# Kernel optimization log

Measured on AMD Instinct MI355X. Metric: run time of the kernel, lower is better.

## Reference

```python
import jax, jax.numpy as jnp
import numpy as np
import itertools

N, F, R, O, OUT = 131072, 32, 256, 5, 100
K = 9  # 2*exp_param + 1 with exp_param=4


def setup_inputs() -> dict:
    key = jax.random.key(0)
    k1, k2, k3 = jax.random.split(key, 3)
    # binary features -> get_route(x)==1 -> categorical rule path
    x = jax.random.randint(k1, (N, F), 0, 2).astype(jnp.float32)
    # first R combinations of O feature indices out of F (itertools order, as in __init__)
    combs = np.array(list(itertools.islice(itertools.combinations(range(F), O), R)), dtype=np.int32)
    comb_space = jax.random.normal(k2, (O, R), dtype=jnp.float32)
    w_out = jax.random.normal(k3, (OUT, R), dtype=jnp.float32) * 0.05
    b_out = jnp.zeros((OUT,), jnp.float32)
    return {"x": x, "comb_space": comb_space, "w_out": w_out, "b_out": b_out,
            "comb_idx": jnp.asarray(combs)}


def reference(x, comb_space, w_out, b_out, comb_idx):
    # Fused version of the per-rule Python loop:
    # gather all rule feature subsets at once: [N, R, O]
    gathered = x[:, comb_idx]
    # per-rule dot product with its parameter vector comb_space[:, r]
    scores = jnp.einsum('nro,or->nr', gathered, comb_space)  # [N, R]
    # polyClip activation: clamp(s^k, -1, 1)
    comb_pred = jnp.clip(scores ** K, -1.0, 1.0)
    # dropout p=0.1 is identity in eval mode
    attn = jax.nn.softmax(comb_pred, axis=1)                 # [N, R]
    out = attn @ w_out.T + b_out                             # [N, OUT]
    return jax.nn.log_softmax(out, axis=1)
```

## Files before the change

kernel.cpp:

```cpp
#include <hip/hip_runtime.h>

typedef unsigned short u16;
typedef _Float16 f16;
typedef __attribute__((ext_vector_type(8))) _Float16 f16x8;
typedef __attribute__((ext_vector_type(4))) _Float16 f16x4;
typedef __attribute__((ext_vector_type(4))) float f32x4;

#define N_ROWS 131072
#define FDIM 32
#define RDIM 256
#define ODIM 5
#define NOUT 100
#define JT 7
#define WAVES 8
#define ROWS_PER_BLOCK (WAVES * 2 * 16)
#define NBLOCKS (N_ROWS / ROWS_PER_BLOCK)

__device__ __forceinline__ u16 f2h_bits(float f) {
    f16 h = (f16)f;
    union { f16 h; u16 u; } v; v.h = h;
    return v.u;
}

__global__ void build_mfrag(const float* __restrict__ cs, const int* __restrict__ ci,
                            u16* __restrict__ mf) {
    int t = blockIdx.x * blockDim.x + threadIdx.x;
    if (t >= 16 * 64) return;
    int lane = t & 63;
    int rt = t >> 6;
    int r = rt * 16 + (lane & 15);
    int kbase = (lane >> 4) * 8;
#pragma unroll
    for (int e = 0; e < 8; ++e) {
        int k = kbase + e;
        float v = 0.f;
#pragma unroll
        for (int o = 0; o < ODIM; ++o)
            if (ci[r * ODIM + o] == k) v = cs[o * RDIM + r];
        mf[t * 8 + e] = f2h_bits(v);
    }
}

__global__ void build_wfrag(const float* __restrict__ w, u16* __restrict__ wf) {
    int t = blockIdx.x * blockDim.x + threadIdx.x;
    if (t >= JT * 8 * 64) return;
    int lane = t & 63;
    int ft = t >> 6;
    int jt = ft >> 3, rtp = ft & 7;
    int j = jt * 16 + (lane & 15);
#pragma unroll
    for (int half = 0; half < 2; ++half) {
#pragma unroll
        for (int e = 0; e < 4; ++e) {
            int r = rtp * 32 + half * 16 + (lane >> 4) * 4 + e;
            float v = (j < NOUT) ? w[j * RDIM + r] : ((j == NOUT) ? 1.0f : 0.0f);
            wf[(ft * 64 + lane) * 8 + half * 4 + e] = f2h_bits(v);
        }
    }
}

__device__ __forceinline__ f16x4 elemop(f32x4 cc) {
    f16x4 r;
#pragma unroll
    for (int i = 0; i < 4; ++i) {
        float s = cc[i];
        float s2 = s * s, s4 = s2 * s2, s8 = s4 * s4;
        float p = fminf(fmaxf(s8 * s, -1.f), 1.f);
        r[i] = (f16)__expf(p);
    }
    return r;
}

__device__ __forceinline__ void epilogue(const f32x4* acc, const float* bv,
                                         int rowbase, int c15, int g,
                                         float* __restrict__ out) {
    float rin[4];
#pragma unroll
    for (int i = 0; i < 4; ++i) rin[i] = 1.f / __shfl(acc[6][i], g * 16 + 4, 64);
#pragma unroll
    for (int i = 0; i < 4; ++i) {
        float lg[JT];
        float mx = -3.0e38f;
#pragma unroll
        for (int jt = 0; jt < JT; ++jt) {
            bool valid = (jt < 6) || (c15 < 4);
            lg[jt] = valid ? (acc[jt][i] * rin[i] + bv[jt]) : -3.0e38f;
            mx = fmaxf(mx, lg[jt]);
        }
#pragma unroll
        for (int m = 1; m <= 8; m <<= 1) mx = fmaxf(mx, __shfl_xor(mx, m, 64));
        float se = 0.f;
#pragma unroll
        for (int jt = 0; jt < JT; ++jt) {
            bool valid = (jt < 6) || (c15 < 4);
            if (valid) se += __expf(lg[jt] - mx);
        }
#pragma unroll
        for (int m = 1; m <= 8; m <<= 1) se += __shfl_xor(se, m, 64);
        float lse = __logf(se);
        int row = rowbase + g * 4 + i;
        float* op = out + (size_t)row * NOUT;
#pragma unroll
        for (int jt = 0; jt < JT; ++jt) {
            bool valid = (jt < 6) || (c15 < 4);
            if (valid) op[jt * 16 + c15] = lg[jt] - mx - lse;
        }
    }
}

__global__ __launch_bounds__(WAVES * 64, 2) void hornet_main(
    const float* __restrict__ x, const u16* __restrict__ mfg,
    const u16* __restrict__ wfg, const float* __restrict__ b_out,
    float* __restrict__ out)
{
    __shared__ __align__(16) u16 wf[JT * 8 * 64 * 8];

    const int tid = threadIdx.x;
    const int lane = tid & 63;
    const int wid = tid >> 6;
    const int c15 = lane & 15, g = lane >> 4;

    const int rowb0 = blockIdx.x * ROWS_PER_BLOCK + wid * 32;
    const float* xp0 = x + (size_t)(rowb0 + c15) * FDIM + g * 8;
    float4 x0a = ((const float4*)xp0)[0];
    float4 x0b = ((const float4*)xp0)[1];
    float4 x1a = ((const float4*)(xp0 + 16 * FDIM))[0];
    float4 x1b = ((const float4*)(xp0 + 16 * FDIM))[1];

    {
        const uint4* wsrc = (const uint4*)wfg;
        uint4* wd = (uint4*)wf;
#pragma unroll
        for (int i = 0; i < 7; ++i) wd[tid + i * 512] = wsrc[tid + i * 512];
    }

    f16x8 a1_0, a1_1;
    a1_0[0] = (f16)x0a.x; a1_0[1] = (f16)x0a.y; a1_0[2] = (f16)x0a.z; a1_0[3] = (f16)x0a.w;
    a1_0[4] = (f16)x0b.x; a1_0[5] = (f16)x0b.y; a1_0[6] = (f16)x0b.z; a1_0[7] = (f16)x0b.w;
    a1_1[0] = (f16)x1a.x; a1_1[1] = (f16)x1a.y; a1_1[2] = (f16)x1a.z; a1_1[3] = (f16)x1a.w;
    a1_1[4] = (f16)x1b.x; a1_1[5] = (f16)x1b.y; a1_1[6] = (f16)x1b.z; a1_1[7] = (f16)x1b.w;

    __syncthreads();

    const f16x8* mfgv = (const f16x8*)mfg;
    const f16x8* wfv = (const f16x8*)wf;

    f32x4 acc0[JT], acc1[JT];
#pragma unroll
    for (int jt = 0; jt < JT; ++jt) {
        acc0[jt] = (f32x4){0.f, 0.f, 0.f, 0.f};
        acc1[jt] = (f32x4){0.f, 0.f, 0.f, 0.f};
    }

#pragma unroll 1
    for (int rtp = 0; rtp < 8; ++rtp) {
        f16x8 b1a = mfgv[(2 * rtp) * 64 + lane];
        f16x8 b1b = mfgv[(2 * rtp + 1) * 64 + lane];
        const f32x4 z = {0.f, 0.f, 0.f, 0.f};
        f32x4 cc0a = __builtin_amdgcn_mfma_f32_16x16x32_f16(b1a, a1_0, z, 0, 0, 0);
        f32x4 cc0b = __builtin_amdgcn_mfma_f32_16x16x32_f16(b1b, a1_0, z, 0, 0, 0);
        f32x4 cc1a = __builtin_amdgcn_mfma_f32_16x16x32_f16(b1a, a1_1, z, 0, 0, 0);
        f32x4 cc1b = __builtin_amdgcn_mfma_f32_16x16x32_f16(b1b, a1_1, z, 0, 0, 0);

        f16x4 a2lo0 = elemop(cc0a);
        f16x4 a2hi0 = elemop(cc0b);
        f16x4 a2lo1 = elemop(cc1a);
        f16x4 a2hi1 = elemop(cc1b);

        const f16x8* wrow = wfv + rtp * 64 + lane;
#pragma unroll
        for (int jt = 0; jt < JT; ++jt) {
            f16x8 b2 = wrow[jt * 8 * 64];
            f16x4 b2lo = __builtin_shufflevector(b2, b2, 0, 1, 2, 3);
            f16x4 b2hi = __builtin_shufflevector(b2, b2, 4, 5, 6, 7);
            acc0[jt] = __builtin_amdgcn_mfma_f32_16x16x16f16(a2lo0, b2lo, acc0[jt], 0, 0, 0);
            acc0[jt] = __builtin_amdgcn_mfma_f32_16x16x16f16(a2hi0, b2hi, acc0[jt], 0, 0, 0);
            acc1[jt] = __builtin_amdgcn_mfma_f32_16x16x16f16(a2lo1, b2lo, acc1[jt], 0, 0, 0);
            acc1[jt] = __builtin_amdgcn_mfma_f32_16x16x16f16(a2hi1, b2hi, acc1[jt], 0, 0, 0);
        }
    }

    float bv[JT];
#pragma unroll
    for (int jt = 0; jt < JT; ++jt) {
        int j = jt * 16 + c15;
        bv[jt] = (j < NOUT) ? b_out[j] : 0.f;
    }

    epilogue(acc0, bv, rowb0, c15, g, out);
    epilogue(acc1, bv, rowb0 + 16, c15, g, out);
}

extern "C" void kernel_launch(void* const* d_in, const int* in_sizes, int n_in,
                              void* d_out, int out_size, void* d_ws, size_t ws_size,
                              hipStream_t stream) {
    const float* x  = (const float*)d_in[0];
    const float* cs = (const float*)d_in[1];
    const float* w  = (const float*)d_in[2];
    const float* b  = (const float*)d_in[3];
    const int*   ci = (const int*)d_in[4];

    u16* mfg = (u16*)d_ws;
    u16* wfg = mfg + 16 * 64 * 8;

    hipLaunchKernelGGL(build_mfrag, dim3(4), dim3(256), 0, stream, cs, ci, mfg);
    hipLaunchKernelGGL(build_wfrag, dim3(14), dim3(256), 0, stream, w, wfg);
    hipLaunchKernelGGL(hornet_main, dim3(NBLOCKS), dim3(WAVES * 64), 0, stream,
                       x, mfg, wfg, b, (float*)d_out);
}
```

Baseline: 38.55 us.

## Fuse fragment-building prep kernels into main kernel and use fast intrinsics

Drops the two small prep kernels that built the f16 MFMA fragments for the rule matrix and output weights. Each block of the main kernel now builds those fragments straight into shared memory from the raw inputs, and the rule fragment is read from LDS instead of global memory. This removes two kernel launches and their dependency gaps, at the cost of every block redoing the gather and conversion work and using more LDS. It also replaces clamp with fmed3, uses packed round-toward-zero f16 conversion, and uses a hardware reciprocal.

```diff
diff --git a/kernel.cpp b/kernel.cpp
--- a/kernel.cpp
+++ b/kernel.cpp
@@ -2,8 +2,9 @@
 
 typedef unsigned short u16;
 typedef _Float16 f16;
+typedef __attribute__((ext_vector_type(2))) __fp16 hf16x2;
+typedef __attribute__((ext_vector_type(4))) _Float16 f16x4;
 typedef __attribute__((ext_vector_type(8))) _Float16 f16x8;
-typedef __attribute__((ext_vector_type(4))) _Float16 f16x4;
 typedef __attribute__((ext_vector_type(4))) float f32x4;
 
 #define N_ROWS 131072
@@ -22,53 +23,21 @@
     return v.u;
 }
 
-__global__ void build_mfrag(const float* __restrict__ cs, const int* __restrict__ ci,
-                            u16* __restrict__ mf) {
-    int t = blockIdx.x * blockDim.x + threadIdx.x;
-    if (t >= 16 * 64) return;
-    int lane = t & 63;
-    int rt = t >> 6;
-    int r = rt * 16 + (lane & 15);
-    int kbase = (lane >> 4) * 8;
-#pragma unroll
-    for (int e = 0; e < 8; ++e) {
-        int k = kbase + e;
-        float v = 0.f;
-#pragma unroll
-        for (int o = 0; o < ODIM; ++o)
-            if (ci[r * ODIM + o] == k) v = cs[o * RDIM + r];
-        mf[t * 8 + e] = f2h_bits(v);
-    }
-}
-
-__global__ void build_wfrag(const float* __restrict__ w, u16* __restrict__ wf) {
-    int t = blockIdx.x * blockDim.x + threadIdx.x;
-    if (t >= JT * 8 * 64) return;
-    int lane = t & 63;
-    int ft = t >> 6;
-    int jt = ft >> 3, rtp = ft & 7;
-    int j = jt * 16 + (lane & 15);
-#pragma unroll
-    for (int half = 0; half < 2; ++half) {
-#pragma unroll
-        for (int e = 0; e < 4; ++e) {
-            int r = rtp * 32 + half * 16 + (lane >> 4) * 4 + e;
-            float v = (j < NOUT) ? w[j * RDIM + r] : ((j == NOUT) ? 1.0f : 0.0f);
-            wf[(ft * 64 + lane) * 8 + half * 4 + e] = f2h_bits(v);
-        }
-    }
-}
-
 __device__ __forceinline__ f16x4 elemop(f32x4 cc) {
-    f16x4 r;
+    float ev[4];
 #pragma unroll
     for (int i = 0; i < 4; ++i) {
         float s = cc[i];
         float s2 = s * s, s4 = s2 * s2, s8 = s4 * s4;
-        float p = fminf(fmaxf(s8 * s, -1.f), 1.f);
-        r[i] = (f16)__expf(p);
-    }
-    return r;
+        float p = __builtin_amdgcn_fmed3f(s8 * s, -1.f, 1.f);
+        ev[i] = __expf(p);
+    }
+    union { hf16x2 h; unsigned u; } lo, hi;
+    lo.h = __builtin_amdgcn_cvt_pkrtz(ev[0], ev[1]);
+    hi.h = __builtin_amdgcn_cvt_pkrtz(ev[2], ev[3]);
+    union { unsigned u[2]; f16x4 v; } r;
+    r.u[0] = lo.u; r.u[1] = hi.u;
+    return r.v;
 }
 
 __device__ __forceinline__ void epilogue(const f32x4* acc, const float* bv,
@@ -76,7 +45,8 @@
                                          float* __restrict__ out) {
     float rin[4];
 #pragma unroll
-    for (int i = 0; i < 4; ++i) rin[i] = 1.f / __shfl(acc[6][i], g * 16 + 4, 64);
+    for (int i = 0; i < 4; ++i)
+        rin[i] = __builtin_amdgcn_rcpf(__shfl(acc[6][i], g * 16 + 4, 64));
 #pragma unroll
     for (int i = 0; i < 4; ++i) {
         float lg[JT];
@@ -109,10 +79,11 @@
 }
 
 __global__ __launch_bounds__(WAVES * 64, 2) void hornet_main(
-    const float* __restrict__ x, const u16* __restrict__ mfg,
-    const u16* __restrict__ wfg, const float* __restrict__ b_out,
-    float* __restrict__ out)
+    const float* __restrict__ x, const float* __restrict__ cs,
+    const float* __restrict__ w, const float* __restrict__ b_out,
+    const int* __restrict__ ci, float* __restrict__ out)
 {
+    __shared__ __align__(16) u16 mf[16 * 64 * 8];
     __shared__ __align__(16) u16 wf[JT * 8 * 64 * 8];
 
     const int tid = threadIdx.x;
@@ -127,11 +98,51 @@
     float4 x1a = ((const float4*)(xp0 + 16 * FDIM))[0];
     float4 x1b = ((const float4*)(xp0 + 16 * FDIM))[1];
 
-    {
-        const uint4* wsrc = (const uint4*)wfg;
-        uint4* wd = (uint4*)wf;
-#pragma unroll
-        for (int i = 0; i < 7; ++i) wd[tid + i * 512] = wsrc[tid + i * 512];
+#pragma unroll
+    for (int ii = 0; ii < 2; ++ii) {
+        int s = tid + ii * 512;
+        int l = s & 63, rt = s >> 6;
+        int r = rt * 16 + (l & 15);
+        int kbase = (l >> 4) * 8;
+        int idx0 = ci[r * ODIM + 0], idx1 = ci[r * ODIM + 1], idx2 = ci[r * ODIM + 2];
+        int idx3 = ci[r * ODIM + 3], idx4 = ci[r * ODIM + 4];
+        u16 vals[8];
+#pragma unroll
+        for (int e = 0; e < 8; ++e) {
+            int k = kbase + e;
+            float v = 0.f;
+            if (idx0 == k) v = cs[0 * RDIM + r];
+            if (idx1 == k) v = cs[1 * RDIM + r];
+            if (idx2 == k) v = cs[2 * RDIM + r];
+            if (idx3 == k) v = cs[3 * RDIM + r];
+            if (idx4 == k) v = cs[4 * RDIM + r];
+            vals[e] = f2h_bits(v);
+        }
+        *(uint4*)(mf + s * 8) = *(const uint4*)vals;
+    }
+
+#pragma unroll
+    for (int ii = 0; ii < 7; ++ii) {
+        int s = tid + ii * 512;
+        int l = s & 63, ft = s >> 6;
+        int jt = ft >> 3, rtp = ft & 7;
+        int j = jt * 16 + (l & 15);
+        u16 vals[8];
+        if (j < NOUT) {
+            const float* wp = w + (size_t)j * RDIM + rtp * 32 + (l >> 4) * 4;
+            float4 va = *(const float4*)wp;
+            float4 vb = *(const float4*)(wp + 16);
+            vals[0] = f2h_bits(va.x); vals[1] = f2h_bits(va.y);
+            vals[2] = f2h_bits(va.z); vals[3] = f2h_bits(va.w);
+            vals[4] = f2h_bits(vb.x); vals[5] = f2h_bits(vb.y);
+            vals[6] = f2h_bits(vb.z); vals[7] = f2h_bits(vb.w);
+        } else {
+            u16 one = f2h_bits(1.0f);
+            u16 fill = (j == NOUT) ? one : (u16)0;
+#pragma unroll
+            for (int e = 0; e < 8; ++e) vals[e] = fill;
+        }
+        *(uint4*)(wf + s * 8) = *(const uint4*)vals;
     }
 
     f16x8 a1_0, a1_1;
@@ -142,7 +153,7 @@
 
     __syncthreads();
 
-    const f16x8* mfgv = (const f16x8*)mfg;
+    const f16x8* mfv = (const f16x8*)mf;
     const f16x8* wfv = (const f16x8*)wf;
 
     f32x4 acc0[JT], acc1[JT];
@@ -154,8 +165,8 @@
 
 #pragma unroll 1
     for (int rtp = 0; rtp < 8; ++rtp) {
-        f16x8 b1a = mfgv[(2 * rtp) * 64 + lane];
-        f16x8 b1b = mfgv[(2 * rtp + 1) * 64 + lane];
+        f16x8 b1a = mfv[(2 * rtp) * 64 + lane];
+        f16x8 b1b = mfv[(2 * rtp + 1) * 64 + lane];
         const f32x4 z = {0.f, 0.f, 0.f, 0.f};
         f32x4 cc0a = __builtin_amdgcn_mfma_f32_16x16x32_f16(b1a, a1_0, z, 0, 0, 0);
         f32x4 cc0b = __builtin_amdgcn_mfma_f32_16x16x32_f16(b1b, a1_0, z, 0, 0, 0);
@@ -200,11 +211,6 @@
     const float* b  = (const float*)d_in[3];
     const int*   ci = (const int*)d_in[4];
 
-    u16* mfg = (u16*)d_ws;
-    u16* wfg = mfg + 16 * 64 * 8;
-
-    hipLaunchKernelGGL(build_mfrag, dim3(4), dim3(256), 0, stream, cs, ci, mfg);
-    hipLaunchKernelGGL(build_wfrag, dim3(14), dim3(256), 0, stream, w, wfg);
     hipLaunchKernelGGL(hornet_main, dim3(NBLOCKS), dim3(WAVES * 64), 0, stream,
-                       x, mfg, wfg, b, (float*)d_out);
-}
+                       x, cs, w, b, ci, (float*)d_out);
+}
```

New measurement: 35.91 us. -6.9%, faster.
